# Kernel optimization log

Hardware: AMD Instinct MI355X
Metric: run time of the kernel (lower is better)

The kernel has to match this reference:

```python
import jax, jax.numpy as jnp
import numpy as np

N_QUBITS = 16
DEPTH = 8
BATCH = 128
DIM = 2 ** N_QUBITS

# Qubit convention: flat index bit for qubit q is at position (n-1-q) from the LSB,
# i.e. qubit 0 occupies the most-significant axis after reshape(B, 2**q, 2, -1).
# Only per-qubit Z expectations are needed, so any consistent convention is faithful.

_CZ_PHASE = None  # built lazily inside simulate to keep dtype handling local


def _apply_1q_batched(state, mat_b, q):
    # state: [B, DIM] complex64, mat_b: [B, 2, 2] complex, gate on qubit q
    B = state.shape[0]
    st = state.reshape(B, 2 ** q, 2, -1)
    return jnp.einsum('bst,bqtr->bqsr', mat_b, st).reshape(B, DIM)


def _apply_1q(state, mat, q):
    # mat: [2, 2] shared across batch
    B = state.shape[0]
    st = state.reshape(B, 2 ** q, 2, -1)
    return jnp.einsum('st,bqtr->bqsr', mat, st).reshape(B, DIM)


def simulate(x, theta):
    """x: [B, n] float32 encoding angles, theta: [n*depth] float32 weights.
    Returns logits [B, n]: logits[:, i] = <Z on Qiskit-string position i> = <Z_{n-1-i}>."""
    B = x.shape[0]
    state = jnp.zeros((B, DIM), jnp.complex64).at[:, 0].set(1.0)

    # Data-encoding layer: RX(x_q) on each qubit q
    for q in range(N_QUBITS):
        h = x[:, q] * 0.5
        c, s = jnp.cos(h), jnp.sin(h)
        mis = (-1j) * s  # complex64 via weak promotion
        mat = jnp.stack([jnp.stack([c + 0j, mis], -1),
                         jnp.stack([mis, c + 0j], -1)], -2)  # [B,2,2]
        state = _apply_1q_batched(state, mat.astype(jnp.complex64), q)

    cz_phase = jnp.array([[1.0, 1.0], [1.0, -1.0]], jnp.complex64)  # -1 iff both bits = 1
    idx = 0
    for _ in range(DEPTH):
        # RY(theta) layer
        for q in range(N_QUBITS):
            h = theta[idx] * 0.5
            idx += 1
            c, s = jnp.cos(h), jnp.sin(h)
            mat = jnp.stack([jnp.stack([c, -s]), jnp.stack([s, c])]).astype(jnp.complex64)
            state = _apply_1q(state, mat, q)
        # CZ chain on adjacent qubits (q, q+1)
        for q in range(N_QUBITS - 1):
            st = state.reshape(B, 2 ** q, 2, 2, -1)
            state = (st * cz_phase[None, None, :, :, None]).reshape(B, DIM)

    probs = state.real ** 2 + state.imag ** 2  # [B, DIM] float32
    z_exps = []
    for q in range(N_QUBITS):
        p = probs.reshape(B, 2 ** q, 2, -1)
        z_exps.append(p[:, :, 0, :].sum((1, 2)) - p[:, :, 1, :].sum((1, 2)))
    z = jnp.stack(z_exps, axis=-1)  # [B, n], z[:, q] = <Z_q>
    # Observable i = SparsePauliOp('I'*i + 'Z' + ...) acts on Qiskit qubit n-1-i
    return z[:, ::-1].astype(jnp.float32)


def setup_inputs() -> dict:
    key = jax.random.key(0)
    k1, k2 = jax.random.split(key)
    x = jax.random.uniform(k1, (BATCH, N_QUBITS), jnp.float32,
                           minval=-np.pi, maxval=np.pi)
    theta = jax.random.normal(k2, (N_QUBITS * DEPTH,), jnp.float32) * 0.1
    return {"x": x, "theta": theta}


def reference(x, theta):
    return simulate(x, theta)
```

## Files before the change

kernel.cpp:

```cpp
#include <hip/hip_runtime.h>
#include <hip/hip_fp16.h>


#define DEV __device__ __forceinline__
typedef unsigned long long ull;
typedef __attribute__((ext_vector_type(2))) float pk2;

DEV pk2 sp2(float v) { return (pk2){v, v}; }

DEV float2 cmul(float2 a, float2 b) {
    return make_float2(a.x * b.x - a.y * b.y, a.x * b.y + a.y * b.x);
}

DEV float dpp_xor1(float x) {
    return __int_as_float(__builtin_amdgcn_update_dpp(0, __float_as_int(x), 0xB1, 0xF, 0xF, false));
}
DEV float dpp_xor2(float x) {
    return __int_as_float(__builtin_amdgcn_update_dpp(0, __float_as_int(x), 0x4E, 0xF, 0xF, false));
}

template <int MJ>
DEV void ry_v(pk2 (&A)[8], float2 cs) {
    const float C = cs.x, S = cs.y;
#pragma unroll
    for (int j = 0; j < 8; ++j)
        if (!(j & MJ)) {
            pk2 t0 = A[j], t1 = A[j | MJ];
            A[j]      = t0 * sp2(C) - t1 * sp2(S);
            A[j | MJ] = t0 * sp2(S) + t1 * sp2(C);
        }
}
DEV void ry_h(pk2 (&A)[8], float2 cs) {
    const float C = cs.x, S = cs.y;
    const pk2 SN = (pk2){-S, S};
#pragma unroll
    for (int j = 0; j < 8; ++j) {
        pk2 t = A[j];
        A[j] = t * sp2(C) + t.yx * SN;
    }
}
DEV void ry_d1(pk2 (&A)[8], float2 cs, int lane) {
    const float C = cs.x, Sg = (lane & 1) ? cs.y : -cs.y;
#pragma unroll
    for (int j = 0; j < 8; ++j) {
        pk2 p; p.x = dpp_xor1(A[j].x); p.y = dpp_xor1(A[j].y);
        A[j] = A[j] * sp2(C) + p * sp2(Sg);
    }
}
DEV void ry_d2(pk2 (&A)[8], float2 cs, int lane) {
    const float C = cs.x, Sg = ((lane >> 1) & 1) ? cs.y : -cs.y;
#pragma unroll
    for (int j = 0; j < 8; ++j) {
        pk2 p; p.x = dpp_xor2(A[j].x); p.y = dpp_xor2(A[j].y);
        A[j] = A[j] * sp2(C) + p * sp2(Sg);
    }
}
DEV void ry_sh(pk2 (&A)[8], float2 cs, int lane, int lb) {
    const float C = cs.x, Sg = ((lane >> lb) & 1) ? cs.y : -cs.y;
#pragma unroll
    for (int j = 0; j < 8; ++j) {
        pk2 p; p.x = __shfl_xor(A[j].x, 1 << lb); p.y = __shfl_xor(A[j].y, 1 << lb);
        A[j] = A[j] * sp2(C) + p * sp2(Sg);
    }
}
DEV void sgnapply2(pk2 (&A)[8], unsigned W) {
#pragma unroll
    for (int j = 0; j < 8; ++j) {
        unsigned sx = ((W >> (2 * j)) & 1u) << 31;
        unsigned sy = ((W >> (2 * j + 1)) & 1u) << 31;
        A[j].x = __uint_as_float(__float_as_uint(A[j].x) ^ sx);
        A[j].y = __uint_as_float(__float_as_uint(A[j].y) ^ sy);
    }
}

__global__ void qsim_pre(const float* __restrict__ x, const float* __restrict__ theta,
                         float2* __restrict__ tsc, float4* __restrict__ psit) {
    const int t = blockIdx.x * 256 + threadIdx.x;
    if (t < 128) {
        float S, C; sincosf(0.5f * theta[t], &S, &C);
        tsc[t] = make_float2(C, S);
    }
    if (t < 2048) {
        const int b = t >> 4, q = t & 15;
        float sa, ca, SA, CA;
        sincosf(0.5f * x[b * 16 + q], &sa, &ca);
        sincosf(0.5f * theta[q], &SA, &CA);
        psit[t] = make_float4(CA * ca, SA * sa, SA * ca, -CA * sa);
    }
}

constexpr unsigned czV3ampK(int K) {
    unsigned m = 0;
    for (int n = 0; n < 16; ++n) {
        int b3 = (n >> 3) & 1, b2 = (n >> 2) & 1, b1 = (n >> 1) & 1, b0 = n & 1;
        int p = 0;
        if (10 <= 14 - K) p ^= b3 & b2;
        if (11 <= 14 - K) p ^= b2 & b1;
        if (12 <= 14 - K) p ^= b1 & b0;
        m |= (unsigned)(p & 1) << n;
    }
    return m;
}
constexpr unsigned czV2ampK(int K) {
    unsigned m = 0;
    for (int n = 0; n < 16; ++n) {
        int b3 = (n >> 3) & 1, b2 = (n >> 2) & 1, b1 = (n >> 1) & 1, b0 = n & 1;
        int p = 0;
        if (4 <= 14 - K) p ^= b3 & b2;
        if (5 <= 14 - K) p ^= b2 & b1;
        if (6 <= 14 - K) p ^= b1 & b0;
        m |= (unsigned)(p & 1) << n;
    }
    return m;
}
template <int K>
DEV void czV3(pk2 (&A)[8], int lane, unsigned T3) {
    unsigned W = czV3ampK(K);
    if (lane & 1) W ^= 0xFF00u;
    if (T3) W ^= 0xFFFFu;
    sgnapply2(A, W);
}
template <int K>
DEV void czV2(pk2 (&A)[8], int lane) {
    unsigned W = czV2ampK(K);
    if ((lane >> 2) & 1) W ^= 0xFF00u;
    if (K <= 7 && ((lane >> 1) & 1)) W ^= 0xAAAAu;
    const unsigned LL = (unsigned)(lane & (lane >> 1));
    const unsigned msk = (K <= 6) ? 0x1Du : 0x1Cu;
    if (__popc(LL & msk) & 1) sgnapply2(A, W ^ 0xFFFFu);
    else sgnapply2(A, W);
}

#define IDXV2(n) (bV2i ^ ((n) << 2))
#define IDXV3(n) (bV3i | ((n) << 6))
#define TRIP(SRC, DST)                                                       \
    {                                                                        \
        __syncthreads();                                                     \
        _Pragma("unroll") for (int j = 0; j < 8; ++j) {                      \
            X[SRC(2 * j)] = A[j].x; X[SRC(2 * j + 1)] = A[j].y;              \
        }                                                                    \
        __syncthreads();                                                     \
        _Pragma("unroll") for (int j = 0; j < 8; ++j) {                      \
            A[j].x = X[DST(2 * j)]; A[j].y = X[DST(2 * j + 1)];              \
        }                                                                    \
    }

#define WTRIP_V1_TO_V2()                                                     \
    {                                                                        \
        pk2* Xw2 = (pk2*)(X + (w << 10));                                    \
        _Pragma("unroll") for (int j = 0; j < 8; ++j)                        \
            Xw2[(j << 6) | ((Lhi ^ (j & 7)) << 2) | Llo] = A[j];             \
        asm volatile("s_waitcnt lgkmcnt(0)" ::: "memory");                   \
        __builtin_amdgcn_sched_barrier(0);                                   \
        float* Xw = X + (w << 10);                                           \
        const int rb = ((Lhi >> 1) << 7) | (Llo << 1) | (Lhi & 1);           \
        const int rs = (Lhi >> 1) & 7;                                       \
        _Pragma("unroll") for (int j = 0; j < 8; ++j) {                      \
            A[j].x = Xw[rb | (((2 * j) ^ rs) << 3)];                         \
            A[j].y = Xw[rb | (((2 * j + 1) ^ rs) << 3)];                     \
        }                                                                    \
    }
#define WTRIP_V2_TO_V1()                                                     \
    {                                                                        \
        float* Xw = X + (w << 10);                                           \
        const int wb = ((Lhi >> 1) << 7) | (Llo << 1) | (Lhi & 1);           \
        const int wsz = (Lhi >> 1) & 7;                                      \
        _Pragma("unroll") for (int j = 0; j < 8; ++j) {                      \
            Xw[wb | (((2 * j) ^ wsz) << 3)] = A[j].x;                        \
            Xw[wb | (((2 * j + 1) ^ wsz) << 3)] = A[j].y;                    \
        }                                                                    \
        asm volatile("s_waitcnt lgkmcnt(0)" ::: "memory");                   \
        __builtin_amdgcn_sched_barrier(0);                                   \
        pk2* Xw2 = (pk2*)(X + (w << 10));                                    \
        _Pragma("unroll") for (int j = 0; j < 8; ++j)                        \
            A[j] = Xw2[(j << 6) | ((Lhi ^ (j & 7)) << 2) | Llo];             \
    }

__global__ __launch_bounds__(1024, 8) void qsim_p0(const float4* __restrict__ psit,
                                                   const float2* __restrict__ tsc,
                                                   __half* __restrict__ st) {
    const int bx = blockIdx.x;
    const int b = bx >> 2, v = (bx >> 1) & 1, c = bx & 1;
    const int tid = threadIdx.x;
    const int lane = tid & 63, w = tid >> 6;

    __shared__ float X[16384];

    const float4* pb = psit + b * 16;
    float2 common = make_float2(1.f, 0.f);
#pragma unroll
    for (int q = 4; q <= 9; ++q) {
        float4 p = pb[q];
        int bit = (lane >> (9 - q)) & 1;
        common = cmul(common, bit ? make_float2(p.z, p.w) : make_float2(p.x, p.y));
    }
#pragma unroll
    for (int q = 10; q <= 13; ++q) {
        float4 p = pb[q];
        int bit = (w >> (13 - q)) & 1;
        common = cmul(common, bit ? make_float2(p.z, p.w) : make_float2(p.x, p.y));
    }
    {
        float4 p = pb[14];
        common = cmul(common, v ? make_float2(p.z, p.w) : make_float2(p.x, p.y));
    }
    float2 ps0[4], ps1[4];
#pragma unroll
    for (int q = 0; q < 4; ++q) {
        float4 p = pb[q];
        ps0[q] = make_float2(p.x, p.y);
        ps1[q] = make_float2(p.z, p.w);
    }

    pk2 A[8];
#pragma unroll
    for (int m = 0; m < 16; ++m) {
        float2 prod = common;
#pragma unroll
        for (int q = 0; q < 4; ++q) {
            int bit = (m >> (3 - q)) & 1;
            prod = cmul(prod, bit ? ps1[q] : ps0[q]);
        }
        float val = c ? prod.y : prod.x;
        if (m & 1) A[m >> 1].y = val; else A[m >> 1].x = val;
    }

    unsigned Pm = 0;
    const int l5 = (lane >> 5) & 1;
#pragma unroll
    for (int m = 0; m < 16; ++m) {
        int m0 = m & 1, m1 = (m >> 1) & 1, m2 = (m >> 2) & 1, m3 = (m >> 3) & 1;
        int pm = ((m3 & m2) ^ (m2 & m1) ^ (m1 & m0) ^ (m0 & l5)) & 1;
        Pm |= ((unsigned)pm) << m;
    }
    const unsigned Ax = ((unsigned)lane << 5) | ((unsigned)w << 1) | (unsigned)v;
    const unsigned AA = (Ax & (Ax >> 1)) & 0x3FFu;

    auto czP0 = [&](int k) {
        unsigned T = __popc(AA >> (k - 1)) & 1u;
        unsigned Wm = T ? (Pm ^ 0xFFFFu) : Pm;
        sgnapply2(A, Wm);
    };

    const int Lhi = lane >> 2, Llo = lane & 3;
    const int bV2i = (Lhi << 10) | (w << 6) | (Lhi << 2) | Llo;
    const int bV3i = (w << 10) | (lane ^ (w << 2));
    const unsigned B3 = ((unsigned)w << 6) | (unsigned)lane;
    const unsigned T3 = (unsigned)(__popc((B3 & (B3 >> 1)) & 0x1FFu) & 1);

    czP0(1);
    ry_v<4>(A, tsc[16 + 0]); ry_v<2>(A, tsc[16 + 1]); ry_v<1>(A, tsc[16 + 2]); ry_h(A, tsc[16 + 3]);
    ry_d2(A, tsc[16 + 8], lane); ry_d1(A, tsc[16 + 9], lane);
    WTRIP_V1_TO_V2();
    ry_v<4>(A, tsc[16 + 4]); ry_v<2>(A, tsc[16 + 5]); ry_v<1>(A, tsc[16 + 6]); ry_h(A, tsc[16 + 7]);
    TRIP(IDXV2, IDXV3);
    ry_v<4>(A, tsc[16 + 10]); ry_v<2>(A, tsc[16 + 11]); ry_v<1>(A, tsc[16 + 12]); ry_h(A, tsc[16 + 13]);
    czV3<2>(A, lane, T3);
    ry_v<4>(A, tsc[32 + 10]); ry_v<2>(A, tsc[32 + 11]); ry_v<1>(A, tsc[32 + 12]);
    TRIP(IDXV3, IDXV2);
    ry_v<4>(A, tsc[32 + 4]); ry_v<2>(A, tsc[32 + 5]); ry_v<1>(A, tsc[32 + 6]); ry_h(A, tsc[32 + 7]);
    __syncthreads();
    WTRIP_V2_TO_V1();
    ry_v<4>(A, tsc[32 + 0]); ry_v<2>(A, tsc[32 + 1]); ry_v<1>(A, tsc[32 + 2]); ry_h(A, tsc[32 + 3]);
    ry_d2(A, tsc[32 + 8], lane); ry_d1(A, tsc[32 + 9], lane);
    czP0(3);
    ry_v<4>(A, tsc[48 + 0]); ry_v<2>(A, tsc[48 + 1]); ry_v<1>(A, tsc[48 + 2]); ry_h(A, tsc[48 + 3]);
    ry_d2(A, tsc[48 + 8], lane); ry_d1(A, tsc[48 + 9], lane);
    WTRIP_V1_TO_V2();
    ry_v<4>(A, tsc[48 + 4]); ry_v<2>(A, tsc[48 + 5]); ry_v<1>(A, tsc[48 + 6]); ry_h(A, tsc[48 + 7]);
    TRIP(IDXV2, IDXV3);
    ry_v<4>(A, tsc[48 + 10]); ry_v<2>(A, tsc[48 + 11]);
    czV3<4>(A, lane, T3);
    ry_v<4>(A, tsc[64 + 10]);
    TRIP(IDXV3, IDXV2);
    ry_v<4>(A, tsc[64 + 4]); ry_v<2>(A, tsc[64 + 5]); ry_v<1>(A, tsc[64 + 6]); ry_h(A, tsc[64 + 7]);
    __syncthreads();
    WTRIP_V2_TO_V1();
    ry_v<4>(A, tsc[64 + 0]); ry_v<2>(A, tsc[64 + 1]); ry_v<1>(A, tsc[64 + 2]); ry_h(A, tsc[64 + 3]);
    ry_d2(A, tsc[64 + 8], lane); ry_d1(A, tsc[64 + 9], lane);
    czP0(5);
    ry_v<4>(A, tsc[80 + 0]); ry_v<2>(A, tsc[80 + 1]); ry_v<1>(A, tsc[80 + 2]); ry_h(A, tsc[80 + 3]);
    ry_d2(A, tsc[80 + 8], lane); ry_d1(A, tsc[80 + 9], lane);
    WTRIP_V1_TO_V2();
    ry_v<4>(A, tsc[80 + 4]); ry_v<2>(A, tsc[80 + 5]); ry_v<1>(A, tsc[80 + 6]); ry_h(A, tsc[80 + 7]);
    czV2<6>(A, lane);
    ry_v<4>(A, tsc[96 + 4]); ry_v<2>(A, tsc[96 + 5]); ry_v<1>(A, tsc[96 + 6]); ry_h(A, tsc[96 + 7]);
    WTRIP_V2_TO_V1();
    ry_v<4>(A, tsc[96 + 0]); ry_v<2>(A, tsc[96 + 1]); ry_v<1>(A, tsc[96 + 2]); ry_h(A, tsc[96 + 3]);
    ry_d2(A, tsc[96 + 8], lane);
    czP0(7);
    ry_v<4>(A, tsc[112 + 0]); ry_v<2>(A, tsc[112 + 1]); ry_v<1>(A, tsc[112 + 2]); ry_h(A, tsc[112 + 3]);
    WTRIP_V1_TO_V2();
    ry_v<4>(A, tsc[112 + 4]); ry_v<2>(A, tsc[112 + 5]); ry_v<1>(A, tsc[112 + 6]); ry_h(A, tsc[112 + 7]);
    czV2<8>(A, lane);
    WTRIP_V2_TO_V1();

    __half* outp = st + (((size_t)(b * 2 + c)) << 15) + ((size_t)v << 14);
#pragma unroll
    for (int j = 0; j < 8; ++j) {
        outp[((2 * j) << 10) | tid] = __float2half(A[j].x);
        outp[((2 * j + 1) << 10) | tid] = __float2half(A[j].y);
    }
}

template <int K>
constexpr unsigned czmask16() {
    unsigned m = 0;
    for (int n = 0; n < 16; ++n) {
        int n0 = n & 1, n1 = (n >> 1) & 1, n2 = (n >> 2) & 1, n3 = (n >> 3) & 1;
        int p = n1 & n0;
        if (K >= 2) p ^= n2 & n1;
        if (K >= 3) p ^= n3 & n2;
        m |= (unsigned)(p & 1) << n;
    }
    return m;
}

template <int K>
DEV void czp1(pk2 (&A)[8], int lb0, int lb1, int lb2, int lb3) {
    unsigned W = czmask16<K>();
    if (K >= 4 && lb0) W ^= 0xFF00u;
    int T = 0;
    if (K >= 5) T ^= (lb1 & lb0);
    if (K >= 6) T ^= (lb2 & lb1);
    if (K >= 7) T ^= (lb3 & lb2);
    if (T) W ^= 0xFFFFu;
    sgnapply2(A, W);
}

template <int K>
DEV void p1_layer(pk2 (&A)[8], const float2* __restrict__ tsc, int lane) {
    ry_h(A, tsc[(K - 1) * 16 + 15]);
    ry_v<1>(A, tsc[(K - 1) * 16 + 14]);
    if constexpr (K >= 3) ry_v<2>(A, tsc[(K - 1) * 16 + 13]);
    if constexpr (K >= 4) ry_v<4>(A, tsc[(K - 1) * 16 + 12]);
    if constexpr (K >= 5) ry_d1(A, tsc[(K - 1) * 16 + 11], lane);
    if constexpr (K >= 6) ry_d2(A, tsc[(K - 1) * 16 + 10], lane);
    if constexpr (K >= 7) ry_sh(A, tsc[(K - 1) * 16 + 9], lane, 2);
    if constexpr (K >= 8) ry_sh(A, tsc[(K - 1) * 16 + 8], lane, 3);
    if constexpr (K < 8) {
        const int lb0 = lane & 1, lb1 = (lane >> 1) & 1, lb2 = (lane >> 2) & 1, lb3 = (lane >> 3) & 1;
        czp1<K>(A, lb0, lb1, lb2, lb3);
    }
}

__global__ __launch_bounds__(512, 8) void qsim_p1(const float4* __restrict__ psit,
                                                  const float2* __restrict__ tsc,
                                                  const __half* __restrict__ st,
                                                  float* __restrict__ partials) {
    const int blk = blockIdx.x;
    const int b = blk >> 4, J = blk & 15;
    const int tid = threadIdx.x;
    const int lane = tid & 63, Wp = tid >> 6;
    const int c = (Wp >> 2) & 1, q4 = (Wp >> 1) & 1, q5 = Wp & 1;

    __shared__ unsigned int H32[2048];
    __shared__ float red[8][11];

    const unsigned int* G32 = (const unsigned int*)st;
    const int base32 = (b << 15) | (J << 9);
#pragma unroll
    for (int s = 0; s < 4; ++s)
        H32[s * 512 + tid] = G32[base32 | ((s >> 1) << 14) | ((s & 1) << 13) | tid];
    __syncthreads();

    const float4 p15 = psit[b * 16 + 15];
    const float cB0 = c ? p15.y : -p15.y;
    const float cB1 = c ? p15.w : -p15.w;
    const pk2 P0pk = (pk2){p15.x, p15.z};
    const pk2 CBpk = (pk2){cB0, cB1};

    const int laneoff = (((lane >> 1) & 1) << 9) | ((lane & 1) << 8) | ((lane >> 2) & 15);
    const int inch = (q4 << 5) | (q5 << 4) | laneoff;
    const __half* H = (const __half*)H32;

    pk2 A[8];
#pragma unroll
    for (int q12 = 0; q12 < 2; ++q12)
#pragma unroll
        for (int q13 = 0; q13 < 2; ++q13)
#pragma unroll
            for (int q14 = 0; q14 < 2; ++q14) {
                const int o = (q12 << 7) | (q13 << 6) | inch;
                const float rA = __half2float(H[(((c) << 1) | q14) * 1024 + o]);
                const float rB = __half2float(H[(((c ^ 1) << 1) | q14) * 1024 + o]);
                const int j = (q12 << 2) | (q13 << 1) | q14;
                A[j] = P0pk * sp2(rA) + CBpk * sp2(rB);
            }

    {
        const int lb0 = lane & 1, lb1 = (lane >> 1) & 1, lb2 = (lane >> 2) & 1, lb3 = (lane >> 3) & 1;
        czp1<1>(A, lb0, lb1, lb2, lb3);
    }
    p1_layer<2>(A, tsc, lane);
    p1_layer<3>(A, tsc, lane);
    p1_layer<4>(A, tsc, lane);
    p1_layer<5>(A, tsc, lane);
    p1_layer<6>(A, tsc, lane);
    p1_layer<7>(A, tsc, lane);
    p1_layer<8>(A, tsc, lane);

    float Ssum = 0.f, Sq[4] = {0.f, 0.f, 0.f, 0.f};
#pragma unroll
    for (int j = 0; j < 8; ++j) {
        pk2 pv = A[j] * A[j];
        float both = pv.x + pv.y;
        Ssum += both;
        Sq[0] += pv.y;
        if (j & 1) Sq[1] += both;
        if (j & 2) Sq[2] += both;
        if (j & 4) Sq[3] += both;
    }
    float P = Ssum, Bv[6];
#pragma unroll
    for (int d = 0; d < 6; ++d) {
        float t = __shfl_xor(P, 1 << d);
        Bv[d] = ((lane >> d) & 1) ? (t - P) : (P - t);
        P += t;
#pragma unroll
        for (int e = 0; e < 6; ++e)
            if (e < d) Bv[e] += __shfl_xor(Bv[e], 1 << d);
    }
#pragma unroll
    for (int j = 0; j < 4; ++j)
#pragma unroll
        for (int d = 0; d < 6; ++d) Sq[j] += __shfl_xor(Sq[j], 1 << d);

    if (lane == 0) {
        red[Wp][0] = P;
#pragma unroll
        for (int d = 0; d < 6; ++d) red[Wp][1 + d] = Bv[d];
#pragma unroll
        for (int j = 0; j < 4; ++j) red[Wp][7 + j] = Sq[j];
    }
    __syncthreads();
    if (tid < 16) {
        const int i = tid;
        float r = 0.f;
#pragma unroll
        for (int Wt = 0; Wt < 8; ++Wt) {
            const float Av = red[Wt][0];
            if (i < 4)        r += Av - 2.f * red[Wt][7 + i];
            else if (i < 10)  r += red[Wt][1 + (i - 4)];
            else if (i == 10) r += (Wt & 1) ? -Av : Av;
            else if (i == 11) r += ((Wt >> 1) & 1) ? -Av : Av;
            else              r += Av;
        }
        if (i >= 12 && ((J >> (i - 12)) & 1)) r = -r;
        partials[(blk << 4) + i] = r;
    }
}

__global__ void qsim_p2(const float* __restrict__ partials, float* __restrict__ out) {
    const int idx = blockIdx.x * 256 + threadIdx.x;
    if (idx < 2048) {
        const int b = idx >> 4, i = idx & 15;
        float s = 0.f;
#pragma unroll
        for (int g = 0; g < 16; ++g) s += partials[(((b << 4) | g) << 4) + i];
        out[idx] = s;
    }
}

extern "C" void kernel_launch(void* const* d_in, const int* in_sizes, int n_in,
                              void* d_out, int out_size, void* d_ws, size_t ws_size,
                              hipStream_t stream) {
    const float* x = (const float*)d_in[0];
    const float* theta = (const float*)d_in[1];
    float* out = (float*)d_out;
    float* ws = (float*)d_ws;
    __half* st = (__half*)ws;
    float* partials = ws + 8388608;
    float2* tsc = (float2*)(ws + 8388608 + 131072);
    float4* psit = (float4*)(ws + 8388608 + 131072 + 256);

    qsim_pre<<<8, 256, 0, stream>>>(x, theta, tsc, psit);
    qsim_p0<<<512, 1024, 0, stream>>>(psit, tsc, st);
    qsim_p1<<<2048, 512, 0, stream>>>(psit, tsc, st, partials);
    qsim_p2<<<8, 256, 0, stream>>>(partials, out);
}
```

Measured before the change: 89.39 us.

## Fold precompute into p0 and replace final reduction kernel with atomics

Removes the separate trig precompute kernel by having each p0 block compute its own sincos tables in shared memory, with designated blocks writing the values p1 needs to global memory. Also removes the final partial-sum kernel: p1 blocks atomically add their partial expectations into the zeroed output. This cuts two kernel launches in exchange for redundant sincos work per block, a memset launch, and non-deterministic float summation order from the atomics.

```diff
diff --git a/kernel.cpp b/kernel.cpp
--- a/kernel.cpp
+++ b/kernel.cpp
@@ -70,22 +70,6 @@
         unsigned sy = ((W >> (2 * j + 1)) & 1u) << 31;
         A[j].x = __uint_as_float(__float_as_uint(A[j].x) ^ sx);
         A[j].y = __uint_as_float(__float_as_uint(A[j].y) ^ sy);
-    }
-}
-
-__global__ void qsim_pre(const float* __restrict__ x, const float* __restrict__ theta,
-                         float2* __restrict__ tsc, float4* __restrict__ psit) {
-    const int t = blockIdx.x * 256 + threadIdx.x;
-    if (t < 128) {
-        float S, C; sincosf(0.5f * theta[t], &S, &C);
-        tsc[t] = make_float2(C, S);
-    }
-    if (t < 2048) {
-        const int b = t >> 4, q = t & 15;
-        float sa, ca, SA, CA;
-        sincosf(0.5f * x[b * 16 + q], &sa, &ca);
-        sincosf(0.5f * theta[q], &SA, &CA);
-        psit[t] = make_float4(CA * ca, SA * sa, SA * ca, -CA * sa);
     }
 }
 
@@ -176,8 +160,10 @@
             A[j] = Xw2[(j << 6) | ((Lhi ^ (j & 7)) << 2) | Llo];             \
     }
 
-__global__ __launch_bounds__(1024, 8) void qsim_p0(const float4* __restrict__ psit,
-                                                   const float2* __restrict__ tsc,
+__global__ __launch_bounds__(1024, 8) void qsim_p0(const float* __restrict__ x,
+                                                   const float* __restrict__ theta,
+                                                   float2* __restrict__ gtsc,
+                                                   float4* __restrict__ gpsit,
                                                    __half* __restrict__ st) {
     const int bx = blockIdx.x;
     const int b = bx >> 2, v = (bx >> 1) & 1, c = bx & 1;
@@ -185,8 +171,27 @@
     const int lane = tid & 63, w = tid >> 6;
 
     __shared__ float X[16384];
-
-    const float4* pb = psit + b * 16;
+    __shared__ float2 TSs[128];
+    __shared__ float4 PSs[16];
+
+    if (tid < 128) {
+        float S, C; sincosf(0.5f * theta[tid], &S, &C);
+        float2 t2 = make_float2(C, S);
+        TSs[tid] = t2;
+        if (bx == 0) gtsc[tid] = t2;
+    } else if (tid < 144) {
+        const int q = tid - 128;
+        float sa, ca, SA, CA;
+        sincosf(0.5f * x[b * 16 + q], &sa, &ca);
+        sincosf(0.5f * theta[q], &SA, &CA);
+        float4 ps = make_float4(CA * ca, SA * sa, SA * ca, -CA * sa);
+        PSs[q] = ps;
+        if ((bx & 3) == 0 && q == 15) gpsit[b * 16 + 15] = ps;
+    }
+    __syncthreads();
+    const float2* tsc = TSs;
+    const float4* pb = PSs;
+
     float2 common = make_float2(1.f, 0.f);
 #pragma unroll
     for (int q = 4; q <= 9; ++q) {
@@ -347,7 +352,7 @@
 __global__ __launch_bounds__(512, 8) void qsim_p1(const float4* __restrict__ psit,
                                                   const float2* __restrict__ tsc,
                                                   const __half* __restrict__ st,
-                                                  float* __restrict__ partials) {
+                                                  float* __restrict__ out) {
     const int blk = blockIdx.x;
     const int b = blk >> 4, J = blk & 15;
     const int tid = threadIdx.x;
@@ -447,18 +452,7 @@
             else              r += Av;
         }
         if (i >= 12 && ((J >> (i - 12)) & 1)) r = -r;
-        partials[(blk << 4) + i] = r;
-    }
-}
-
-__global__ void qsim_p2(const float* __restrict__ partials, float* __restrict__ out) {
-    const int idx = blockIdx.x * 256 + threadIdx.x;
-    if (idx < 2048) {
-        const int b = idx >> 4, i = idx & 15;
-        float s = 0.f;
-#pragma unroll
-        for (int g = 0; g < 16; ++g) s += partials[(((b << 4) | g) << 4) + i];
-        out[idx] = s;
+        atomicAdd(&out[(b << 4) + i], r);
     }
 }
 
@@ -470,12 +464,10 @@
     float* out = (float*)d_out;
     float* ws = (float*)d_ws;
     __half* st = (__half*)ws;
-    float* partials = ws + 8388608;
-    float2* tsc = (float2*)(ws + 8388608 + 131072);
-    float4* psit = (float4*)(ws + 8388608 + 131072 + 256);
-
-    qsim_pre<<<8, 256, 0, stream>>>(x, theta, tsc, psit);
-    qsim_p0<<<512, 1024, 0, stream>>>(psit, tsc, st);
-    qsim_p1<<<2048, 512, 0, stream>>>(psit, tsc, st, partials);
-    qsim_p2<<<8, 256, 0, stream>>>(partials, out);
-}
+    float2* gtsc = (float2*)(ws + 8388608 + 131072);
+    float4* gpsit = (float4*)(ws + 8388608 + 131072 + 256);
+
+    hipMemsetAsync(d_out, 0, (size_t)out_size * sizeof(float), stream);
+    qsim_p0<<<512, 1024, 0, stream>>>(x, theta, gtsc, gpsit, st);
+    qsim_p1<<<2048, 512, 0, stream>>>(gpsit, gtsc, st, out);
+}
```

Result: no change. 89.73 us (+0.4%).
